# Kernel tuning notes

Hardware: AMD Instinct MI355X
Metric: run time of the kernel (lower is better)

The kernel has to match this reference:

```python
import jax, jax.numpy as jnp
from jax import lax
import numpy as np

D_MODEL = 1024
D_INNER = 2048   # expand=2
D_STATE = 16
D_CONV = 4
DT_RANK = 64     # ceil(1024/16)
N_LAYERS = 24
PATCH = 16
H0 = W0 = 24     # 384 // 16
BATCH = 2
IMG = 384


def setup_inputs() -> dict:
    key = jax.random.key(0)
    ks = jax.random.split(key, 12)
    def rn(k, shape, scale=0.02):
        return jax.random.normal(k, shape, jnp.float32) * scale
    A_init = jnp.broadcast_to(jnp.arange(1, D_STATE + 1, dtype=jnp.float32),
                              (N_LAYERS, D_INNER, D_STATE))
    return {
        "x": jax.random.normal(ks[0], (BATCH, 3, IMG, IMG), jnp.float32),
        "patch_w": rn(ks[1], (D_MODEL, 3, PATCH, PATCH)),
        "patch_b": jnp.zeros((D_MODEL,), jnp.float32),
        "cls_token": rn(ks[2], (1, 1, D_MODEL)),
        "pos_embed": rn(ks[3], (1, 1 + H0 * W0, D_MODEL)),
        "ln_w": jnp.ones((N_LAYERS, D_MODEL), jnp.float32),
        "ln_b": jnp.zeros((N_LAYERS, D_MODEL), jnp.float32),
        "in_proj_w": rn(ks[4], (N_LAYERS, 2 * D_INNER, D_MODEL)),
        "conv_w": rn(ks[5], (N_LAYERS, D_INNER, D_CONV), 0.1),
        "conv_b": jnp.zeros((N_LAYERS, D_INNER), jnp.float32),
        "x_proj_w": rn(ks[6], (N_LAYERS, DT_RANK + 2 * D_STATE, D_INNER)),
        "dt_proj_w": rn(ks[7], (N_LAYERS, D_INNER, DT_RANK), 0.1),
        "dt_proj_b": rn(ks[8], (N_LAYERS, D_INNER), 0.5),
        "A_log": jnp.log(A_init),
        "D_skip": jnp.ones((N_LAYERS, D_INNER), jnp.float32),
        "out_proj_w": rn(ks[9], (N_LAYERS, D_MODEL, D_INNER)),
    }


def _layernorm(x, w, b):
    m = x.mean(-1, keepdims=True)
    xc = x - m
    v = (xc * xc).mean(-1, keepdims=True)
    return xc * lax.rsqrt(v + 1e-5) * w + b


def _mamba_block(tok, p):
    # tok: [B, L, D]
    lw, lb, ipw, cw, cb, xpw, dpw, dpb, alog, dsk, opw = p
    h = _layernorm(tok, lw, lb)
    xz = jnp.einsum('bld,ed->ble', h, ipw)          # [B, L, 2*d_inner]
    xc, z = jnp.split(xz, 2, axis=-1)
    # causal depthwise conv1d over sequence, kernel D_CONV
    u = lax.conv_general_dilated(
        xc.transpose(0, 2, 1), cw[:, None, :], (1,), [(D_CONV - 1, 0)],
        dimension_numbers=('NCH', 'OIH', 'NCH'), feature_group_count=D_INNER)
    u = jax.nn.silu(u + cb[None, :, None]).transpose(0, 2, 1)  # [B, L, d_inner]
    dbl = jnp.einsum('ble,fe->blf', u, xpw)         # [B, L, dt_rank + 2*d_state]
    dt = jax.nn.softplus(jnp.einsum('blr,dr->bld', dbl[..., :DT_RANK], dpw) + dpb)
    Bm = dbl[..., DT_RANK:DT_RANK + D_STATE]        # [B, L, d_state]
    Cm = dbl[..., DT_RANK + D_STATE:]               # [B, L, d_state]
    A = -jnp.exp(alog)                              # [d_inner, d_state]

    def step(hst, inp):
        dt_t, B_t, C_t, u_t = inp                   # [B,d_inner],[B,ds],[B,ds],[B,d_inner]
        hst = jnp.exp(dt_t[..., None] * A) * hst + (dt_t * u_t)[..., None] * B_t[:, None, :]
        y_t = jnp.einsum('bds,bs->bd', hst, C_t)
        return hst, y_t

    h0 = jnp.zeros((tok.shape[0], D_INNER, D_STATE), tok.dtype)
    _, ys = lax.scan(step, h0, (dt.transpose(1, 0, 2), Bm.transpose(1, 0, 2),
                                Cm.transpose(1, 0, 2), u.transpose(1, 0, 2)))
    y = ys.transpose(1, 0, 2) + dsk * u
    y = y * jax.nn.silu(z)
    return tok + jnp.einsum('ble,de->bld', y, opw)


def reference(x, patch_w, patch_b, cls_token, pos_embed, ln_w, ln_b, in_proj_w,
              conv_w, conv_b, x_proj_w, dt_proj_w, dt_proj_b, A_log, D_skip,
              out_proj_w):
    # patch embed: conv stride=kernel=16
    feat = lax.conv_general_dilated(x, patch_w, (PATCH, PATCH), 'VALID',
                                    dimension_numbers=('NCHW', 'OIHW', 'NCHW'))
    feat = feat + patch_b[None, :, None, None]
    B, Dm, H, W = feat.shape
    tokens = feat.reshape(B, Dm, H * W).transpose(0, 2, 1)
    tokens = jnp.concatenate([jnp.broadcast_to(cls_token, (B, 1, Dm)), tokens], 1)
    # bilinear (half-pixel, align_corners=False) pos-embed interpolation
    pp = pos_embed[:, 1:, :].reshape(1, H0, W0, Dm)
    pp = jax.image.resize(pp, (1, H, W, Dm), method='bilinear').reshape(1, H * W, Dm)
    tokens = tokens + jnp.concatenate([pos_embed[:, :1, :], pp], 1)
    params = (ln_w, ln_b, in_proj_w, conv_w, conv_b, x_proj_w, dt_proj_w,
              dt_proj_b, A_log, D_skip, out_proj_w)
    blk = jax.checkpoint(_mamba_block)
    tokens, _ = lax.scan(lambda t, p: (blk(t, p), None), tokens, params)
    return tokens
```

## Files before the change

kernel.cpp:

```cpp
#include <hip/hip_runtime.h>
#include <hip/hip_bf16.h>
#include <math.h>

#define BATCH 2
#define LSEQ 577
#define DM 1024
#define DI 2048
#define DSTATE 16
#define DTR 64
#define NLAYERS 24
#define NP 576
#define MROWS 1154
#define NC 32
#define LC 19
#define LOG2E 1.4426950408889634f

typedef __attribute__((ext_vector_type(8))) short short8v;
typedef __attribute__((ext_vector_type(4))) float f32x4;

__device__ __forceinline__ ushort f2bf(float f) {
  unsigned int b = __float_as_uint(f);
  return (ushort)((b + 0x7FFFu + ((b >> 16) & 1u)) >> 16);
}
__device__ __forceinline__ float bf2f(ushort u) {
  return __uint_as_float(((unsigned int)u) << 16);
}
__device__ __forceinline__ void gload16(const void* g, void* l) {
  __builtin_amdgcn_global_load_lds(
      (const __attribute__((address_space(1))) unsigned int*)g,
      (__attribute__((address_space(3))) unsigned int*)l, 16, 0, 0);
}
__device__ __forceinline__ void cvt16(const float* g, char* ldsrow, int bb, int bswz) {
  float4 v0 = *(const float4*)(g);
  float4 v1 = *(const float4*)(g + 4);
  float4 v2 = *(const float4*)(g + 8);
  float4 v3 = *(const float4*)(g + 12);
  short8v c0 = {(short)f2bf(v0.x), (short)f2bf(v0.y), (short)f2bf(v0.z), (short)f2bf(v0.w),
                (short)f2bf(v1.x), (short)f2bf(v1.y), (short)f2bf(v1.z), (short)f2bf(v1.w)};
  short8v c1 = {(short)f2bf(v2.x), (short)f2bf(v2.y), (short)f2bf(v2.z), (short)f2bf(v2.w),
                (short)f2bf(v3.x), (short)f2bf(v3.y), (short)f2bf(v3.z), (short)f2bf(v3.w)};
  *(short8v*)(ldsrow + (bb ^ bswz)) = c0;
  *(short8v*)(ldsrow + ((bb + 16) ^ bswz)) = c1;
}

#define SEG0 786432u
#define SEG1 4718592u
#define SEG2 3145728u
#define SEG3 50331648u
#define SEG4 100663296u
#define CUM1 (SEG0)
#define CUM2 (CUM1+SEG1)
#define CUM3 (CUM2+SEG2)
#define CUM4 (CUM3+SEG3)
#define CUMT (CUM4+SEG4)
#define F2BF_BLOCKS (CUMT/4096)

__global__ void f2bf_all_k(const float* __restrict__ i0, const float* __restrict__ i1,
                           const float* __restrict__ i2, const float* __restrict__ i3,
                           const float* __restrict__ i4,
                           ushort* __restrict__ o0, ushort* __restrict__ o1,
                           ushort* __restrict__ o2, ushort* __restrict__ o3,
                           ushort* __restrict__ o4) {
  size_t base = (size_t)blockIdx.x * 4096;
  const float* in; ushort* out; size_t off;
  if (base < CUM1)      { in = i0; out = o0; off = base; }
  else if (base < CUM2) { in = i1; out = o1; off = base - CUM1; }
  else if (base < CUM3) { in = i2; out = o2; off = base - CUM2; }
  else if (base < CUM4) { in = i3; out = o3; off = base - CUM3; }
  else                  { in = i4; out = o4; off = base - CUM4; }
  size_t p = off + threadIdx.x * 4;
  #pragma unroll
  for (int j = 0; j < 4; ++j) {
    float4 v = *(const float4*)(in + p + j * 1024);
    ushort4 o;
    o.x = f2bf(v.x); o.y = f2bf(v.y); o.z = f2bf(v.z); o.w = f2bf(v.w);
    *(ushort4*)(out + p + j * 1024) = o;
  }
}

template<int AF32, int MODE>
__global__ __launch_bounds__(256) void gemm64(
    const void* __restrict__ Ap_, int lda,
    const ushort* __restrict__ Bw, int ldb,
    float* __restrict__ C, int ldc,
    int M, int N, int K,
    const float* __restrict__ bias, const float* __restrict__ pos,
    ushort* __restrict__ o16a, ushort* __restrict__ o16b)
{
  __shared__ char lds[AF32 ? 24576 : 49152];
  int tid = threadIdx.x;
  int lane = tid & 63, w = tid >> 6;

  int nwg = gridDim.x * gridDim.y;
  int f = blockIdx.y * gridDim.x + blockIdx.x;
  int L = (f & 7) * (nwg >> 3) + (f >> 3);
  int bx = L % gridDim.x, by = L / gridDim.x;
  int bm = by * 64, bn = bx * 128;

  int srow = tid >> 3;
  int scol = ((tid & 7) ^ (srow & 7)) << 3;

  const ushort* gb0 = Bw + (size_t)(bn + srow) * ldb + scol;
  const ushort* gb1 = Bw + (size_t)(bn + 32 + srow) * ldb + scol;
  const ushort* gb2 = Bw + (size_t)(bn + 64 + srow) * ldb + scol;
  const ushort* gb3 = Bw + (size_t)(bn + 96 + srow) * ldb + scol;

  const ushort* ga0 = nullptr; const ushort* ga1 = nullptr;
  const float* gAf = nullptr; char* ldsArow = nullptr; int bb = 0, bswz = 0;
  if (!AF32) {
    const ushort* Abf = (const ushort*)Ap_;
    int ra0 = bm + srow;      if (ra0 > M - 1) ra0 = M - 1;
    int ra1 = bm + 32 + srow; if (ra1 > M - 1) ra1 = M - 1;
    ga0 = Abf + (size_t)ra0 * lda + scol;
    ga1 = Abf + (size_t)ra1 * lda + scol;
  } else {
    int brow = tid >> 2;
    int be0 = (tid & 3) << 4;
    bb = be0 << 1; bswz = (brow & 7) << 4;
    int raf = bm + brow; if (raf > M - 1) raf = M - 1;
    gAf = (const float*)Ap_ + (size_t)raf * lda + be0;
    ldsArow = lds + brow * 128;
  }

  int wr = w >> 1, wc = w & 1;
  int fr = lane & 15;
  int fsw = (fr & 7) << 4;
  int fk = (lane >> 4) << 4;

  f32x4 acc[2][4];
  #pragma unroll
  for (int m = 0; m < 2; ++m)
    #pragma unroll
    for (int n = 0; n < 4; ++n) acc[m][n] = (f32x4){0.f, 0.f, 0.f, 0.f};

  if constexpr (!AF32) {
    auto stage = [&](int buf, int k0) {
      char* p = lds + buf * 24576;
      gload16(ga0 + k0, p + (w << 10));
      gload16(ga1 + k0, p + 4096 + (w << 10));
      gload16(gb0 + k0, p + 8192 + (w << 10));
      gload16(gb1 + k0, p + 12288 + (w << 10));
      gload16(gb2 + k0, p + 16384 + (w << 10));
      gload16(gb3 + k0, p + 20480 + (w << 10));
    };
    int nk = K >> 6;
    stage(0, 0);
    for (int k = 0; k < nk; ++k) {
      int cur = k & 1;
      if (k + 1 < nk) {
        stage(cur ^ 1, (k + 1) << 6);
        asm volatile("s_waitcnt vmcnt(6)" ::: "memory");
      } else {
        asm volatile("s_waitcnt vmcnt(0)" ::: "memory");
      }
      __builtin_amdgcn_s_barrier();
      char* p = lds + cur * 24576;
      #pragma unroll
      for (int ks = 0; ks < 2; ++ks) {
        int cb = (ks * 64 + fk) ^ fsw;
        short8v af[2], bf[4];
        #pragma unroll
        for (int m = 0; m < 2; ++m)
          af[m] = *(const short8v*)(p + (wr * 32 + m * 16 + fr) * 128 + cb);
        #pragma unroll
        for (int n = 0; n < 4; ++n)
          bf[n] = *(const short8v*)(p + 8192 + (wc * 64 + n * 16 + fr) * 128 + cb);
        #pragma unroll
        for (int m = 0; m < 2; ++m)
          #pragma unroll
          for (int n = 0; n < 4; ++n)
            acc[m][n] = __builtin_amdgcn_mfma_f32_16x16x32_bf16(af[m], bf[n], acc[m][n], 0, 0, 0);
      }
      __builtin_amdgcn_s_barrier();
    }
  } else {
    for (int k0 = 0; k0 < K; k0 += 64) {
      cvt16(gAf + k0, ldsArow, bb, bswz);
      gload16(gb0 + k0, lds + 8192 + (w << 10));
      gload16(gb1 + k0, lds + 12288 + (w << 10));
      gload16(gb2 + k0, lds + 16384 + (w << 10));
      gload16(gb3 + k0, lds + 20480 + (w << 10));
      __syncthreads();
      #pragma unroll
      for (int ks = 0; ks < 2; ++ks) {
        int cb = (ks * 64 + fk) ^ fsw;
        short8v af[2], bf[4];
        #pragma unroll
        for (int m = 0; m < 2; ++m)
          af[m] = *(const short8v*)(lds + (wr * 32 + m * 16 + fr) * 128 + cb);
        #pragma unroll
        for (int n = 0; n < 4; ++n)
          bf[n] = *(const short8v*)(lds + 8192 + (wc * 64 + n * 16 + fr) * 128 + cb);
        #pragma unroll
        for (int m = 0; m < 2; ++m)
          #pragma unroll
          for (int n = 0; n < 4; ++n)
            acc[m][n] = __builtin_amdgcn_mfma_f32_16x16x32_bf16(af[m], bf[n], acc[m][n], 0, 0, 0);
      }
      __syncthreads();
    }
  }

  #pragma unroll
  for (int m = 0; m < 2; ++m) {
    int rb = bm + wr * 32 + m * 16 + ((lane >> 4) << 2);
    #pragma unroll
    for (int j = 0; j < 4; ++j) {
      int r = rb + j;
      if (r >= M) break;
      #pragma unroll
      for (int n2 = 0; n2 < 4; ++n2) {
        int n = bn + wc * 64 + n2 * 16 + fr;
        float v = acc[m][n2][j];
        if (MODE == 1) {
          C[(size_t)r * ldc + n] += v;
        } else if (MODE == 3) {
          int b = r / NP, p = r % NP;
          C[((size_t)(b * LSEQ + 1 + p)) * ldc + n] = v + bias[n] + pos[(size_t)(1 + p) * ldc + n];
        } else if (MODE == 4) {
          if (n < DI) o16a[(size_t)r * DI + n] = f2bf(v);
          else        o16b[(size_t)r * DI + n - DI] = f2bf(v);
        } else {
          float t = v + bias[n];
          o16a[(size_t)r * N + n] = f2bf((t > 20.f) ? t : log1pf(__expf(t)));
        }
      }
    }
  }
}

__global__ __launch_bounds__(256) void xproj_k(
    const ushort* __restrict__ A, const ushort* __restrict__ W,
    float* __restrict__ C, int M)
{
  __shared__ char lds[40960];
  int tid = threadIdx.x;
  int lane = tid & 63, w = tid >> 6;
  int bm = blockIdx.y * 64;
  int kbase = blockIdx.x * 256;

  int srow = tid >> 3;
  int scol = ((tid & 7) ^ (srow & 7)) << 3;
  int ra0 = bm + srow;      if (ra0 > M - 1) ra0 = M - 1;
  int ra1 = bm + 32 + srow; if (ra1 > M - 1) ra1 = M - 1;
  const ushort* ga0 = A + (size_t)ra0 * DI + kbase + scol;
  const ushort* ga1 = A + (size_t)ra1 * DI + kbase + scol;
  const ushort* gb0 = W + (size_t)(srow)      * DI + kbase + scol;
  const ushort* gb1 = W + (size_t)(srow + 32) * DI + kbase + scol;
  const ushort* gb2 = W + (size_t)(srow + 64) * DI + kbase + scol;

  int fr = lane & 15;
  int fsw = (fr & 7) << 4;
  int fk = (lane >> 4) << 4;
  int arow = (w * 16 + fr) * 128;

  f32x4 acc[6];
  #pragma unroll
  for (int n = 0; n < 6; ++n) acc[n] = (f32x4){0.f, 0.f, 0.f, 0.f};

  auto stage = [&](int buf, int k0) {
    char* p = lds + buf * 20480;
    gload16(ga0 + k0, p + (w << 10));
    gload16(ga1 + k0, p + 4096 + (w << 10));
    gload16(gb0 + k0, p + 8192 + (w << 10));
    gload16(gb1 + k0, p + 12288 + (w << 10));
    gload16(gb2 + k0, p + 16384 + (w << 10));
  };
  stage(0, 0);
  #pragma unroll
  for (int k = 0; k < 4; ++k) {
    int cur = k & 1;
    if (k + 1 < 4) {
      stage(cur ^ 1, (k + 1) << 6);
      asm volatile("s_waitcnt vmcnt(5)" ::: "memory");
    } else {
      asm volatile("s_waitcnt vmcnt(0)" ::: "memory");
    }
    __builtin_amdgcn_s_barrier();
    char* p = lds + cur * 20480;
    #pragma unroll
    for (int ks = 0; ks < 2; ++ks) {
      int cb = (ks * 64 + fk) ^ fsw;
      short8v af = *(const short8v*)(p + arow + cb);
      #pragma unroll
      for (int n = 0; n < 6; ++n) {
        short8v bf = *(const short8v*)(p + 8192 + (n * 16 + fr) * 128 + cb);
        acc[n] = __builtin_amdgcn_mfma_f32_16x16x32_bf16(af, bf, acc[n], 0, 0, 0);
      }
    }
    __builtin_amdgcn_s_barrier();
  }

  int rb = bm + w * 16 + ((lane >> 4) << 2);
  #pragma unroll
  for (int j = 0; j < 4; ++j) {
    int r = rb + j;
    if (r >= M) break;
    #pragma unroll
    for (int n = 0; n < 6; ++n)
      atomicAdd(C + (size_t)r * 96 + n * 16 + fr, acc[n][j]);
  }
}

__global__ void im2col_k(const float* __restrict__ x, ushort* __restrict__ patches) {
  int idx = blockIdx.x * 256 + threadIdx.x;
  if (idx >= BATCH * NP * 768) return;
  int col = idx % 768, row = idx / 768;
  int b = row / NP, p = row % NP;
  int ph = p / 24, pw = p % 24;
  int c = col >> 8, r = col & 255, kh = r >> 4, kw = r & 15;
  patches[idx] = f2bf(x[(((size_t)(b * 3 + c) * 384) + ph * 16 + kh) * 384 + pw * 16 + kw]);
}

__global__ void cls_k(const float* __restrict__ cls, const float* __restrict__ pos,
                      float* __restrict__ out) {
  int n = blockIdx.x * 256 + threadIdx.x;
  if (n >= DM) return;
  float v = cls[n] + pos[n];
  out[n] = v;
  out[(size_t)LSEQ * DM + n] = v;
}

__global__ __launch_bounds__(256) void ln_k(const float* __restrict__ tok,
    const float* __restrict__ w, const float* __restrict__ bsh,
    ushort* __restrict__ h, float* __restrict__ dbl0) {
  int row = blockIdx.x;
  const float* xr = tok + (size_t)row * DM;
  int tid = threadIdx.x;
  if (tid < 96) dbl0[(size_t)row * 96 + tid] = 0.f;
  float v[4];
  #pragma unroll
  for (int i = 0; i < 4; ++i) v[i] = xr[tid + 256 * i];
  float s = v[0] + v[1] + v[2] + v[3];
  float s2 = v[0] * v[0] + v[1] * v[1] + v[2] * v[2] + v[3] * v[3];
  #pragma unroll
  for (int off = 32; off; off >>= 1) { s += __shfl_xor(s, off); s2 += __shfl_xor(s2, off); }
  __shared__ float ps[4], ps2[4];
  if ((tid & 63) == 0) { ps[tid >> 6] = s; ps2[tid >> 6] = s2; }
  __syncthreads();
  s = ps[0] + ps[1] + ps[2] + ps[3];
  s2 = ps2[0] + ps2[1] + ps2[2] + ps2[3];
  float mean = s * (1.f / DM);
  float var = s2 * (1.f / DM) - mean * mean;
  float inv = rsqrtf(var + 1e-5f);
  #pragma unroll
  for (int i = 0; i < 4; ++i) {
    int c = tid + 256 * i;
    h[(size_t)row * DM + c] = f2bf((v[i] - mean) * inv * w[c] + bsh[c]);
  }
}

__global__ void conv_silu_k(const ushort* __restrict__ xc, const float* __restrict__ cw,
                            const float* __restrict__ cb, ushort* __restrict__ ubf) {
  int idx = blockIdx.x * 256 + threadIdx.x;
  if (idx >= MROWS * (DI / 2)) return;
  int d2 = idx & (DI / 2 - 1);
  int ro = idx >> 10;
  int l = ro % LSEQ;
  int d = d2 << 1;
  float a0 = cb[d], a1 = cb[d + 1];
  const uint* xrow = (const uint*)xc + d2;
  float2 w0 = *(const float2*)(cw + d * 4);
  float2 w1 = *(const float2*)(cw + d * 4 + 2);
  float2 w2 = *(const float2*)(cw + (d + 1) * 4);
  float2 w3 = *(const float2*)(cw + (d + 1) * 4 + 2);
  float wA[4] = {w0.x, w0.y, w1.x, w1.y};
  float wB[4] = {w2.x, w2.y, w3.x, w3.y};
  #pragma unroll
  for (int k = 0; k < 4; ++k) {
    int ll = l - 3 + k;
    if (ll >= 0) {
      uint pr = xrow[(size_t)(ro - 3 + k) * (DI / 2)];
      a0 += bf2f((ushort)(pr & 0xFFFFu)) * wA[k];
      a1 += bf2f((ushort)(pr >> 16)) * wB[k];
    }
  }
  uint outp = (uint)f2bf(a0 / (1.f + __expf(-a0))) |
              ((uint)f2bf(a1 / (1.f + __expf(-a1))) << 16);
  ((uint*)ubf)[idx] = outp;
}

__global__ __launch_bounds__(256) void scan1_k(
    const ushort* __restrict__ dt, const ushort* __restrict__ ubf,
    const float* __restrict__ dbl, const float* __restrict__ alog,
    ushort* __restrict__ Ap, ushort* __restrict__ He)
{
  int d = blockIdx.x * 256 + threadIdx.x;
  int b = blockIdx.y, c = blockIdx.z;
  int t0 = c * LC, t1 = t0 + LC; if (t1 > LSEQ) t1 = LSEQ;
  float Ad[DSTATE], h[DSTATE];
  #pragma unroll
  for (int s = 0; s < DSTATE; ++s) {
    Ad[s] = -__expf(alog[d * DSTATE + s]); h[s] = 0.f;
  }
  bool fast = true;
  #pragma unroll
  for (int s = 1; s < DSTATE; ++s)
    fast = fast && (fabsf(Ad[s] - (s + 1) * Ad[0]) <= 1e-5f * (s + 1) * fabsf(Ad[0]));
  size_t o = (((size_t)(b * NC + c)) * DI + d) * DSTATE;
  if (fast) {
    float a1 = Ad[0] * LOG2E;
    float p = 1.f;
    for (int t = t0; t < t1; ++t) {
      size_t ro = (size_t)b * LSEQ + t;
      float dtv = bf2f(dt[ro * DI + d]);
      float du = dtv * bf2f(ubf[ro * DI + d]);
      const float* r = dbl + ro * 96;
      float e1 = exp2f(dtv * a1);
      p *= e1;
      float e = e1;
      #pragma unroll
      for (int s = 0; s < DSTATE; ++s) {
        h[s] = e * h[s] + du * r[64 + s];
        e *= e1;
      }
    }
    float pw = p;
    #pragma unroll
    for (int s = 0; s < DSTATE; ++s) {
      Ap[o + s] = f2bf(pw); He[o + s] = f2bf(h[s]);
      pw *= p;
    }
  } else {
    float ap[DSTATE];
    #pragma unroll
    for (int s = 0; s < DSTATE; ++s) ap[s] = 1.f;
    for (int t = t0; t < t1; ++t) {
      size_t ro = (size_t)b * LSEQ + t;
      float dtv = bf2f(dt[ro * DI + d]);
      float du = dtv * bf2f(ubf[ro * DI + d]);
      const float* r = dbl + ro * 96;
      #pragma unroll
      for (int s = 0; s < DSTATE; ++s) {
        float e = __expf(dtv * Ad[s]);
        h[s] = e * h[s] + du * r[64 + s];
        ap[s] *= e;
      }
    }
    #pragma unroll
    for (int s = 0; s < DSTATE; ++s) { Ap[o + s] = f2bf(ap[s]); He[o + s] = f2bf(h[s]); }
  }
}

__global__ __launch_bounds__(256) void scan2_k(
    ushort* __restrict__ Ap, const ushort* __restrict__ He)
{
  int ds = blockIdx.x * 256 + threadIdx.x;
  int b = blockIdx.y;
  float h = 0.f;
  #pragma unroll
  for (int g = 0; g < NC; g += 8) {
    float apg[8], heg[8];
    #pragma unroll
    for (int j = 0; j < 8; ++j) {
      size_t oo = ((size_t)(b * NC + g + j)) * DI * DSTATE + ds;
      apg[j] = bf2f(Ap[oo]); heg[j] = bf2f(He[oo]);
    }
    #pragma unroll
    for (int j = 0; j < 8; ++j) {
      size_t oo = ((size_t)(b * NC + g + j)) * DI * DSTATE + ds;
      Ap[oo] = f2bf(h);
      h = apg[j] * h + heg[j];
    }
  }
}

__global__ __launch_bounds__(256) void scan3_k(
    const ushort* __restrict__ dt, const ushort* __restrict__ ubf,
    const float* __restrict__ dbl, const ushort* __restrict__ zbf,
    const float* __restrict__ alog, const float* __restrict__ dsk,
    const ushort* __restrict__ H0, ushort* __restrict__ y)
{
  int d = blockIdx.x * 256 + threadIdx.x;
  int b = blockIdx.y, c = blockIdx.z;
  int t0 = c * LC, t1 = t0 + LC; if (t1 > LSEQ) t1 = LSEQ;
  float Ad[DSTATE], h[DSTATE];
  size_t o = (((size_t)(b * NC + c)) * DI + d) * DSTATE;
  #pragma unroll
  for (int s = 0; s < DSTATE; ++s) {
    Ad[s] = -__expf(alog[d * DSTATE + s]);
    h[s] = bf2f(H0[o + s]);
  }
  bool fast = true;
  #pragma unroll
  for (int s = 1; s < DSTATE; ++s)
    fast = fast && (fabsf(Ad[s] - (s + 1) * Ad[0]) <= 1e-5f * (s + 1) * fabsf(Ad[0]));
  float Dv = dsk[d];
  if (fast) {
    float a1 = Ad[0] * LOG2E;
    for (int t = t0; t < t1; ++t) {
      size_t ro = (size_t)b * LSEQ + t;
      float dtv = bf2f(dt[ro * DI + d]);
      float uv = bf2f(ubf[ro * DI + d]);
      float du = dtv * uv;
      const float* r = dbl + ro * 96;
      float e1 = exp2f(dtv * a1);
      float e = e1;
      float yv = 0.f;
      #pragma unroll
      for (int s = 0; s < DSTATE; ++s) {
        h[s] = e * h[s] + du * r[64 + s];
        yv += h[s] * r[80 + s];
        e *= e1;
      }
      float z = bf2f(zbf[ro * DI + d]);
      y[ro * DI + d] = f2bf((yv + Dv * uv) * (z / (1.f + __expf(-z))));
    }
  } else {
    for (int t = t0; t < t1; ++t) {
      size_t ro = (size_t)b * LSEQ + t;
      float dtv = bf2f(dt[ro * DI + d]);
      float uv = bf2f(ubf[ro * DI + d]);
      float du = dtv * uv;
      const float* r = dbl + ro * 96;
      float yv = 0.f;
      #pragma unroll
      for (int s = 0; s < DSTATE; ++s) {
        h[s] = __expf(dtv * Ad[s]) * h[s] + du * r[64 + s];
        yv += h[s] * r[80 + s];
      }
      float z = bf2f(zbf[ro * DI + d]);
      y[ro * DI + d] = f2bf((yv + Dv * uv) * (z / (1.f + __expf(-z))));
    }
  }
}

extern "C" void kernel_launch(void* const* d_in, const int* in_sizes, int n_in,
                              void* d_out, int out_size, void* d_ws, size_t ws_size,
                              hipStream_t stream) {
  const float* x         = (const float*)d_in[0];
  const float* patch_w   = (const float*)d_in[1];
  const float* patch_b   = (const float*)d_in[2];
  const float* cls_token = (const float*)d_in[3];
  const float* pos_embed = (const float*)d_in[4];
  const float* ln_w      = (const float*)d_in[5];
  const float* ln_b      = (const float*)d_in[6];
  const float* in_proj_w = (const float*)d_in[7];
  const float* conv_w    = (const float*)d_in[8];
  const float* conv_b    = (const float*)d_in[9];
  const float* x_proj_w  = (const float*)d_in[10];
  const float* dt_proj_w = (const float*)d_in[11];
  const float* dt_proj_b = (const float*)d_in[12];
  const float* A_log     = (const float*)d_in[13];
  const float* D_skip    = (const float*)d_in[14];
  const float* out_proj_w= (const float*)d_in[15];
  float* tok = (float*)d_out;

  char* base = (char*)d_ws;
  ushort* xc_bf  = (ushort*)(base);
  ushort* z_bf   = (ushort*)(base + 4726784);
  ushort* u_bf   = (ushort*)(base + 9453568);
  float*  dbl    = (float*)(base + 14180352);
  ushort* dt_bf  = (ushort*)(base + 14623488);
  ushort* h_bf   = (ushort*)(base + 19350272);
  ushort* y_bf   = (ushort*)(base + 21713664);
  ushort* Ap     = (ushort*)(base + 26440448);
  ushort* He     = (ushort*)(base + 30634752);
  ushort* wpatch = (ushort*)(base + 34829056);
  ushort* wxp    = (ushort*)(base + 36401920);
  ushort* wdt    = (ushort*)(base + 45839104);
  ushort* wout   = (ushort*)(base + 52130560);
  ushort* win    = (ushort*)(base + 152793856);
  ushort* patches= (ushort*)u_bf;

  f2bf_all_k<<<F2BF_BLOCKS, 256, 0, stream>>>(patch_w, x_proj_w, dt_proj_w, out_proj_w,
                                              in_proj_w, wpatch, wxp, wdt, wout, win);

  im2col_k<<<(BATCH * NP * 768 + 255) / 256, 256, 0, stream>>>(x, patches);
  {
    dim3 gp(DM / 128, (BATCH * NP) / 64);
    gemm64<0, 3><<<gp, 256, 0, stream>>>(patches, 768, wpatch, 768, tok, DM,
                                         BATCH * NP, DM, 768, patch_b, pos_embed,
                                         nullptr, nullptr);
  }
  cls_k<<<(DM + 255) / 256, 256, 0, stream>>>(cls_token, pos_embed, tok);

  for (int l = 0; l < NLAYERS; ++l) {
    ln_k<<<MROWS, 256, 0, stream>>>(tok, ln_w + l * DM, ln_b + l * DM, h_bf, dbl);

    {
      dim3 g1(2 * DI / 128, (MROWS + 63) / 64);
      gemm64<0, 4><<<g1, 256, 0, stream>>>(h_bf, DM, win + (size_t)l * 2 * DI * DM, DM,
                                           nullptr, 0, MROWS, 2 * DI, DM,
                                           nullptr, nullptr, xc_bf, z_bf);
    }

    conv_silu_k<<<(MROWS * (DI / 2) + 255) / 256, 256, 0, stream>>>(
        xc_bf, conv_w + (size_t)l * DI * 4, conv_b + (size_t)l * DI, u_bf);

    {
      dim3 g2(8, (MROWS + 63) / 64);
      xproj_k<<<g2, 256, 0, stream>>>(u_bf, wxp + (size_t)l * 96 * DI, dbl, MROWS);
    }

    {
      dim3 g3(DI / 128, (MROWS + 63) / 64);
      gemm64<1, 5><<<g3, 256, 0, stream>>>(dbl, 96, wdt + (size_t)l * DI * DTR, DTR,
                                           nullptr, 0, MROWS, DI, DTR,
                                           dt_proj_b + (size_t)l * DI, nullptr, dt_bf, nullptr);
    }

    {
      dim3 gs(DI / 256, BATCH, NC);
      scan1_k<<<gs, 256, 0, stream>>>(dt_bf, u_bf, dbl,
                                      A_log + (size_t)l * DI * DSTATE, Ap, He);
      dim3 gs2(DI * DSTATE / 256, BATCH);
      scan2_k<<<gs2, 256, 0, stream>>>(Ap, He);
      scan3_k<<<gs, 256, 0, stream>>>(dt_bf, u_bf, dbl, z_bf,
                                      A_log + (size_t)l * DI * DSTATE, D_skip + (size_t)l * DI,
                                      Ap, y_bf);
    }

    {
      dim3 g4(DM / 128, (MROWS + 63) / 64);
      gemm64<0, 1><<<g4, 256, 0, stream>>>(y_bf, DI, wout + (size_t)l * DM * DI, DI,
                                           tok, DM, MROWS, DM, DI, nullptr, nullptr,
                                           nullptr, nullptr);
    }
  }
}
```

Before: 2.900 ms.

## Convert in_proj and out_proj weights to bf16 inside the GEMM load path

Removes the upfront f32-to-bf16 conversion pass over the large in_proj and out_proj weight tensors, about 150M elements read and written once per call. A new BF32 GEMM variant instead loads f32 B tiles into registers, converts them and writes them to swizzled LDS, with register prefetch double-buffering. The cost is twice the global bytes for B inside each GEMM, since every M-tile re-reads the f32 weights, plus conversion ALU work and synchronous LDS writes in the main loop.

```diff
diff --git a/kernel.cpp b/kernel.cpp
--- a/kernel.cpp
+++ b/kernel.cpp
@@ -46,28 +46,20 @@
 #define SEG0 786432u
 #define SEG1 4718592u
 #define SEG2 3145728u
-#define SEG3 50331648u
-#define SEG4 100663296u
 #define CUM1 (SEG0)
 #define CUM2 (CUM1+SEG1)
-#define CUM3 (CUM2+SEG2)
-#define CUM4 (CUM3+SEG3)
-#define CUMT (CUM4+SEG4)
+#define CUMT (CUM2+SEG2)
 #define F2BF_BLOCKS (CUMT/4096)
 
 __global__ void f2bf_all_k(const float* __restrict__ i0, const float* __restrict__ i1,
-                           const float* __restrict__ i2, const float* __restrict__ i3,
-                           const float* __restrict__ i4,
+                           const float* __restrict__ i2,
                            ushort* __restrict__ o0, ushort* __restrict__ o1,
-                           ushort* __restrict__ o2, ushort* __restrict__ o3,
-                           ushort* __restrict__ o4) {
+                           ushort* __restrict__ o2) {
   size_t base = (size_t)blockIdx.x * 4096;
   const float* in; ushort* out; size_t off;
   if (base < CUM1)      { in = i0; out = o0; off = base; }
   else if (base < CUM2) { in = i1; out = o1; off = base - CUM1; }
-  else if (base < CUM3) { in = i2; out = o2; off = base - CUM2; }
-  else if (base < CUM4) { in = i3; out = o3; off = base - CUM3; }
-  else                  { in = i4; out = o4; off = base - CUM4; }
+  else                  { in = i2; out = o2; off = base - CUM2; }
   size_t p = off + threadIdx.x * 4;
   #pragma unroll
   for (int j = 0; j < 4; ++j) {
@@ -78,10 +70,10 @@
   }
 }
 
-template<int AF32, int MODE>
+template<int AF32, int BF32, int MODE>
 __global__ __launch_bounds__(256) void gemm64(
     const void* __restrict__ Ap_, int lda,
-    const ushort* __restrict__ Bw, int ldb,
+    const void* __restrict__ Bw_, int ldb,
     float* __restrict__ C, int ldc,
     int M, int N, int K,
     const float* __restrict__ bias, const float* __restrict__ pos,
@@ -100,10 +92,19 @@
   int srow = tid >> 3;
   int scol = ((tid & 7) ^ (srow & 7)) << 3;
 
-  const ushort* gb0 = Bw + (size_t)(bn + srow) * ldb + scol;
-  const ushort* gb1 = Bw + (size_t)(bn + 32 + srow) * ldb + scol;
-  const ushort* gb2 = Bw + (size_t)(bn + 64 + srow) * ldb + scol;
-  const ushort* gb3 = Bw + (size_t)(bn + 96 + srow) * ldb + scol;
+  const ushort* gb0 = nullptr; const ushort* gb1 = nullptr;
+  const ushort* gb2 = nullptr; const ushort* gb3 = nullptr;
+  const float* gBf = nullptr; int brow32 = 0, bhalf = 0, bswzB = 0;
+  if constexpr (!BF32) {
+    const ushort* Bw = (const ushort*)Bw_;
+    gb0 = Bw + (size_t)(bn + srow) * ldb + scol;
+    gb1 = Bw + (size_t)(bn + 32 + srow) * ldb + scol;
+    gb2 = Bw + (size_t)(bn + 64 + srow) * ldb + scol;
+    gb3 = Bw + (size_t)(bn + 96 + srow) * ldb + scol;
+  } else {
+    brow32 = tid >> 1; bhalf = tid & 1; bswzB = (brow32 & 7) << 4;
+    gBf = (const float*)Bw_ + (size_t)(bn + brow32) * ldb + bhalf * 32;
+  }
 
   const ushort* ga0 = nullptr; const ushort* ga1 = nullptr;
   const float* gAf = nullptr; char* ldsArow = nullptr; int bb = 0, bswz = 0;
@@ -133,7 +134,60 @@
     #pragma unroll
     for (int n = 0; n < 4; ++n) acc[m][n] = (f32x4){0.f, 0.f, 0.f, 0.f};
 
-  if constexpr (!AF32) {
+  #define MFMA_STEP(p)                                                          \
+    _Pragma("unroll")                                                           \
+    for (int ks = 0; ks < 2; ++ks) {                                            \
+      int cb = (ks * 64 + fk) ^ fsw;                                            \
+      short8v af[2], bf[4];                                                     \
+      _Pragma("unroll")                                                         \
+      for (int m = 0; m < 2; ++m)                                               \
+        af[m] = *(const short8v*)((p) + (wr * 32 + m * 16 + fr) * 128 + cb);    \
+      _Pragma("unroll")                                                         \
+      for (int n = 0; n < 4; ++n)                                               \
+        bf[n] = *(const short8v*)((p) + 8192 + (wc * 64 + n * 16 + fr) * 128 + cb); \
+      _Pragma("unroll")                                                         \
+      for (int m = 0; m < 2; ++m)                                               \
+        _Pragma("unroll")                                                       \
+        for (int n = 0; n < 4; ++n)                                             \
+          acc[m][n] = __builtin_amdgcn_mfma_f32_16x16x32_bf16(af[m], bf[n], acc[m][n], 0, 0, 0); \
+    }
+
+  if constexpr (BF32) {
+    float4 rb[8];
+    auto stageA = [&](int buf, int k0) {
+      char* p = lds + buf * 24576;
+      gload16(ga0 + k0, p + (w << 10));
+      gload16(ga1 + k0, p + 4096 + (w << 10));
+    };
+    auto loadB = [&](int k0) {
+      #pragma unroll
+      for (int j = 0; j < 8; ++j) rb[j] = *(const float4*)(gBf + k0 + j * 4);
+    };
+    auto writeB = [&](int buf) {
+      char* prow = lds + buf * 24576 + 8192 + brow32 * 128;
+      int bb0 = bhalf * 64;
+      #pragma unroll
+      for (int j = 0; j < 4; ++j) {
+        float4 v0 = rb[2 * j], v1 = rb[2 * j + 1];
+        short8v c = {(short)f2bf(v0.x), (short)f2bf(v0.y), (short)f2bf(v0.z), (short)f2bf(v0.w),
+                     (short)f2bf(v1.x), (short)f2bf(v1.y), (short)f2bf(v1.z), (short)f2bf(v1.w)};
+        *(short8v*)(prow + ((bb0 + j * 16) ^ bswzB)) = c;
+      }
+    };
+    int nk = K >> 6;
+    stageA(0, 0);
+    loadB(0);
+    writeB(0);
+    __syncthreads();
+    for (int k = 0; k < nk; ++k) {
+      int cur = k & 1;
+      if (k + 1 < nk) { stageA(cur ^ 1, (k + 1) << 6); loadB((k + 1) << 6); }
+      char* p = lds + cur * 24576;
+      MFMA_STEP(p)
+      if (k + 1 < nk) writeB(cur ^ 1);
+      __syncthreads();
+    }
+  } else if constexpr (!AF32) {
     auto stage = [&](int buf, int k0) {
       char* p = lds + buf * 24576;
       gload16(ga0 + k0, p + (w << 10));
@@ -155,22 +209,7 @@
       }
       __builtin_amdgcn_s_barrier();
       char* p = lds + cur * 24576;
-      #pragma unroll
-      for (int ks = 0; ks < 2; ++ks) {
-        int cb = (ks * 64 + fk) ^ fsw;
-        short8v af[2], bf[4];
-        #pragma unroll
-        for (int m = 0; m < 2; ++m)
-          af[m] = *(const short8v*)(p + (wr * 32 + m * 16 + fr) * 128 + cb);
-        #pragma unroll
-        for (int n = 0; n < 4; ++n)
-          bf[n] = *(const short8v*)(p + 8192 + (wc * 64 + n * 16 + fr) * 128 + cb);
-        #pragma unroll
-        for (int m = 0; m < 2; ++m)
-          #pragma unroll
-          for (int n = 0; n < 4; ++n)
-            acc[m][n] = __builtin_amdgcn_mfma_f32_16x16x32_bf16(af[m], bf[n], acc[m][n], 0, 0, 0);
-      }
+      MFMA_STEP(p)
       __builtin_amdgcn_s_barrier();
     }
   } else {
@@ -181,32 +220,19 @@
       gload16(gb2 + k0, lds + 16384 + (w << 10));
       gload16(gb3 + k0, lds + 20480 + (w << 10));
       __syncthreads();
-      #pragma unroll
-      for (int ks = 0; ks < 2; ++ks) {
-        int cb = (ks * 64 + fk) ^ fsw;
-        short8v af[2], bf[4];
-        #pragma unroll
-        for (int m = 0; m < 2; ++m)
-          af[m] = *(const short8v*)(lds + (wr * 32 + m * 16 + fr) * 128 + cb);
-        #pragma unroll
-        for (int n = 0; n < 4; ++n)
-          bf[n] = *(const short8v*)(lds + 8192 + (wc * 64 + n * 16 + fr) * 128 + cb);
-        #pragma unroll
-        for (int m = 0; m < 2; ++m)
-          #pragma unroll
-          for (int n = 0; n < 4; ++n)
-            acc[m][n] = __builtin_amdgcn_mfma_f32_16x16x32_bf16(af[m], bf[n], acc[m][n], 0, 0, 0);
-      }
+      char* p = lds;
+      MFMA_STEP(p)
       __syncthreads();
     }
   }
+  #undef MFMA_STEP
 
   #pragma unroll
   for (int m = 0; m < 2; ++m) {
-    int rb = bm + wr * 32 + m * 16 + ((lane >> 4) << 2);
+    int rb2 = bm + wr * 32 + m * 16 + ((lane >> 4) << 2);
     #pragma unroll
     for (int j = 0; j < 4; ++j) {
-      int r = rb + j;
+      int r = rb2 + j;
       if (r >= M) break;
       #pragma unroll
       for (int n2 = 0; n2 < 4; ++n2) {
@@ -559,19 +585,17 @@
   ushort* wpatch = (ushort*)(base + 34829056);
   ushort* wxp    = (ushort*)(base + 36401920);
   ushort* wdt    = (ushort*)(base + 45839104);
-  ushort* wout   = (ushort*)(base + 52130560);
-  ushort* win    = (ushort*)(base + 152793856);
   ushort* patches= (ushort*)u_bf;
 
-  f2bf_all_k<<<F2BF_BLOCKS, 256, 0, stream>>>(patch_w, x_proj_w, dt_proj_w, out_proj_w,
-                                              in_proj_w, wpatch, wxp, wdt, wout, win);
+  f2bf_all_k<<<F2BF_BLOCKS, 256, 0, stream>>>(patch_w, x_proj_w, dt_proj_w,
+                                              wpatch, wxp, wdt);
 
   im2col_k<<<(BATCH * NP * 768 + 255) / 256, 256, 0, stream>>>(x, patches);
   {
     dim3 gp(DM / 128, (BATCH * NP) / 64);
-    gemm64<0, 3><<<gp, 256, 0, stream>>>(patches, 768, wpatch, 768, tok, DM,
-                                         BATCH * NP, DM, 768, patch_b, pos_embed,
-                                         nullptr, nullptr);
+    gemm64<0, 0, 3><<<gp, 256, 0, stream>>>(patches, 768, wpatch, 768, tok, DM,
+                                            BATCH * NP, DM, 768, patch_b, pos_embed,
+                                            nullptr, nullptr);
   }
   cls_k<<<(DM + 255) / 256, 256, 0, stream>>>(cls_token, pos_embed, tok);
 
@@ -580,9 +604,9 @@
 
     {
       dim3 g1(2 * DI / 128, (MROWS + 63) / 64);
-      gemm64<0, 4><<<g1, 256, 0, stream>>>(h_bf, DM, win + (size_t)l * 2 * DI * DM, DM,
-                                           nullptr, 0, MROWS, 2 * DI, DM,
-                                           nullptr, nullptr, xc_bf, z_bf);
+      gemm64<0, 1, 4><<<g1, 256, 0, stream>>>(h_bf, DM, in_proj_w + (size_t)l * 2 * DI * DM, DM,
+                                              nullptr, 0, MROWS, 2 * DI, DM,
+                                              nullptr, nullptr, xc_bf, z_bf);
     }
 
     conv_silu_k<<<(MROWS * (DI / 2) + 255) / 256, 256, 0, stream>>>(
@@ -595,9 +619,9 @@
 
     {
       dim3 g3(DI / 128, (MROWS + 63) / 64);
-      gemm64<1, 5><<<g3, 256, 0, stream>>>(dbl, 96, wdt + (size_t)l * DI * DTR, DTR,
-                                           nullptr, 0, MROWS, DI, DTR,
-                                           dt_proj_b + (size_t)l * DI, nullptr, dt_bf, nullptr);
+      gemm64<1, 0, 5><<<g3, 256, 0, stream>>>(dbl, 96, wdt + (size_t)l * DI * DTR, DTR,
+                                              nullptr, 0, MROWS, DI, DTR,
+                                              dt_proj_b + (size_t)l * DI, nullptr, dt_bf, nullptr);
     }
 
     {
@@ -613,9 +637,9 @@
 
     {
       dim3 g4(DM / 128, (MROWS + 63) / 64);
-      gemm64<0, 1><<<g4, 256, 0, stream>>>(y_bf, DI, wout + (size_t)l * DM * DI, DI,
-                                           tok, DM, MROWS, DM, DI, nullptr, nullptr,
-                                           nullptr, nullptr);
-    }
-  }
-}
+      gemm64<0, 1, 1><<<g4, 256, 0, stream>>>(y_bf, DI, out_proj_w + (size_t)l * DM * DI, DI,
+                                              tok, DM, MROWS, DM, DI, nullptr, nullptr,
+                                              nullptr, nullptr);
+    }
+  }
+}
```

After: 4.570 ms. +57.6%, slower.
